# Optimization experiments

Hardware: AMD Instinct MI355X
Metric: run time of the kernel (lower is better)

## Reference

```python
import jax, jax.numpy as jnp
import numpy as np

HIDDEN = 2048
N_HEADS = 16
HEAD_DIM = HIDDEN // N_HEADS  # 128
ROTARY_DIM = 32
ROPE_BASE = 10000.0
NEG_INF = -10000.0  # matches torch code's additive mask constant


def setup_inputs() -> dict:
    key = jax.random.key(0)
    k1, k2, k3 = jax.random.split(key, 3)
    x = jax.random.normal(k1, (2, 2048, HIDDEN), dtype=jnp.float32)
    # scale weights like nn.Linear default init (uniform ~ 1/sqrt(fan_in))
    Wqkv_w = jax.random.normal(k2, (3 * HIDDEN, HIDDEN), dtype=jnp.float32) * (1.0 / np.sqrt(HIDDEN))
    Wqkv_b = jax.random.normal(k3, (3 * HIDDEN,), dtype=jnp.float32) * 0.01
    return {"x": x, "Wqkv_w": Wqkv_w, "Wqkv_b": Wqkv_b}


def _rope_cos_sin(seqlen, dtype):
    inv_freq = 1.0 / (ROPE_BASE ** (jnp.arange(0, ROTARY_DIM, 2, dtype=jnp.float32) / ROTARY_DIM))
    t = jnp.arange(seqlen, dtype=jnp.float32)
    freqs = jnp.outer(t, inv_freq)  # (S, ROTARY_DIM//2)
    return jnp.cos(freqs).astype(dtype), jnp.sin(freqs).astype(dtype)


def _apply_rotary(u, cos, sin):
    # u: (B, S, H, D); rotate first ROTARY_DIM dims, GPT-NeoX half-split style
    u_rot, u_pass = u[..., :ROTARY_DIM], u[..., ROTARY_DIM:]
    u1, u2 = u_rot[..., : ROTARY_DIM // 2], u_rot[..., ROTARY_DIM // 2 :]
    c = cos[None, :, None, :]  # (1, S, 1, ROTARY_DIM//2)
    s = sin[None, :, None, :]
    rot = jnp.concatenate([u1 * c - u2 * s, u1 * s + u2 * c], axis=-1)
    return jnp.concatenate([rot, u_pass], axis=-1)


def reference(x, Wqkv_w, Wqkv_b):
    B, S, _ = x.shape
    qkv = jnp.einsum("bse,oe->bso", x, Wqkv_w) + Wqkv_b  # (B, S, 3*H*D)
    qkv = qkv.reshape(B, S, 3, N_HEADS, HEAD_DIM)
    cos, sin = _rope_cos_sin(S, x.dtype)
    q = _apply_rotary(qkv[:, :, 0], cos, sin)
    k = _apply_rotary(qkv[:, :, 1], cos, sin)
    v = qkv[:, :, 2]
    scale = 1.0 / np.sqrt(HEAD_DIM)
    scores = jnp.einsum("bthd,bshd->bhts", q, k * scale)  # (B, H, T, S)
    causal_mask = jnp.triu(jnp.full((S, S), NEG_INF, dtype=scores.dtype), 1)
    scores = scores + causal_mask
    attn = jax.nn.softmax(scores, axis=-1)
    out = jnp.einsum("bhts,bshd->bthd", attn, v)  # (B, S, H, D)
    return out.reshape(B, S, N_HEADS * HEAD_DIM)
```

## Files before the change

### kernel.cpp

```cpp
#include <hip/hip_runtime.h>

#define B_    2
#define S_    2048
#define E_    2048
#define NH_   16
#define HD_   128
#define NQKV_ 6144
#define M_    4096
#define XN_   (M_ * E_)
#define NPAN  (E_ / 32)

typedef short bf16x8 __attribute__((ext_vector_type(8)));
typedef float f32x4  __attribute__((ext_vector_type(4)));

typedef const __attribute__((address_space(1))) void* gas_t;
typedef __attribute__((address_space(3))) void*       las_t;

__device__ inline float b2f(unsigned short u) {
    return __uint_as_float(((unsigned int)u) << 16);
}
__device__ inline unsigned short f2b(float f) {
    unsigned int x = __float_as_uint(f);
    x = x + 0x7fffu + ((x >> 16) & 1u);
    return (unsigned short)(x >> 16);
}
__device__ inline unsigned int pk2(float lo, float hi) {
    return (unsigned int)f2b(lo) | ((unsigned int)f2b(hi) << 16);
}

__global__ __launch_bounds__(256) void cvt_bf16(
    const float* __restrict__ X,
    const float* __restrict__ W,
    unsigned short* __restrict__ O)
{
    const long i = (long)(blockIdx.x * 256 + threadIdx.x) * 8;
    const float* src = (i < XN_) ? (X + i) : (W + (i - XN_));
    const float4 a = *(const float4*)(src);
    const float4 b = *(const float4*)(src + 4);
    uint4 o = { pk2(a.x, a.y), pk2(a.z, a.w), pk2(b.x, b.y), pk2(b.z, b.w) };
    *(uint4*)(O + i) = o;
}

__global__ __launch_bounds__(512, 2) void qkv_gemm(
    const unsigned short* __restrict__ Xb,
    const unsigned short* __restrict__ Wb,
    const float* __restrict__ bias,
    unsigned short* __restrict__ qb,
    unsigned short* __restrict__ kb,
    unsigned short* __restrict__ vb)
{
    __shared__ __align__(16) unsigned short As[4][256 * 32];
    __shared__ __align__(16) unsigned short Bs[4][256 * 32];

    const int t    = threadIdx.x;
    const int lane = t & 63;
    const int w    = t >> 6;
    const int wr   = w >> 2;
    const int wc   = w & 3;
    const int quad = (lane >> 4) & 3;
    const int l16  = lane & 15;

    const int wg = ((int)blockIdx.x & 7) * 48 + ((int)blockIdx.x >> 3);
    const int m0 = (wg / 24) * 256;
    const int n0 = (wg % 24) * 256;

    auto stageA = [&](int p) {
        const int sl = p & 3;
        const int k0 = p * 32;
        #pragma unroll
        for (int c = 0; c < 2; c++) {
            const int ub  = c * 512 + w * 64;
            const int u   = ub + lane;
            const int row = u >> 2;
            const int ko  = (u & 3) ^ ((row >> 1) & 3);
            __builtin_amdgcn_global_load_lds(
                (gas_t)(Xb + (size_t)(m0 + row) * E_ + k0 + ko * 8),
                (las_t)&As[sl][ub * 8], 16, 0, 0);
        }
    };
    auto stageB = [&](int p) {
        const int sl = p & 3;
        const int k0 = p * 32;
        #pragma unroll
        for (int c = 0; c < 2; c++) {
            const int ub  = c * 512 + w * 64;
            const int u   = ub + lane;
            const int row = u >> 2;
            const int ko  = (u & 3) ^ ((row >> 1) & 3);
            __builtin_amdgcn_global_load_lds(
                (gas_t)(Wb + (size_t)(n0 + row) * E_ + k0 + ko * 8),
                (las_t)&Bs[sl][ub * 8], 16, 0, 0);
        }
    };

    f32x4 acc[8][4];
    #pragma unroll
    for (int i = 0; i < 8; i++)
        #pragma unroll
        for (int j = 0; j < 4; j++)
            #pragma unroll
            for (int r = 0; r < 4; r++) acc[i][j][r] = 0.0f;

    stageA(0); stageB(0);
    stageA(1); stageB(1);
    stageA(2); stageB(2);
    asm volatile("s_waitcnt vmcnt(0)" ::: "memory");
    __builtin_amdgcn_s_barrier();

    for (int p = 0; p < NPAN; p++) {
        const int sl = p & 3;
        bf16x8 af[4], bf[4];

        #pragma unroll
        for (int mf = 0; mf < 4; mf++) {
            const int row = wr * 128 + mf * 16 + l16;
            af[mf] = *(const bf16x8*)&As[sl][row * 32 + (quad ^ ((row >> 1) & 3)) * 8];
        }
        #pragma unroll
        for (int nf = 0; nf < 4; nf++) {
            const int rb = wc * 64 + nf * 16 + l16;
            bf[nf] = *(const bf16x8*)&Bs[sl][rb * 32 + (quad ^ ((rb >> 1) & 3)) * 8];
        }
        if (p + 3 < NPAN) stageA(p + 3);
        __builtin_amdgcn_s_barrier();
        __builtin_amdgcn_s_setprio(1);
        #pragma unroll
        for (int mf = 0; mf < 4; mf++)
            #pragma unroll
            for (int nf = 0; nf < 4; nf++)
                acc[mf][nf] = __builtin_amdgcn_mfma_f32_16x16x32_bf16(
                    af[mf], bf[nf], acc[mf][nf], 0, 0, 0);
        __builtin_amdgcn_s_setprio(0);
        __builtin_amdgcn_s_barrier();

        #pragma unroll
        for (int mf = 0; mf < 4; mf++) {
            const int row = wr * 128 + 64 + mf * 16 + l16;
            af[mf] = *(const bf16x8*)&As[sl][row * 32 + (quad ^ ((row >> 1) & 3)) * 8];
        }
        if (p + 3 < NPAN) stageB(p + 3);
        asm volatile("s_waitcnt vmcnt(8)" ::: "memory");
        __builtin_amdgcn_s_barrier();
        __builtin_amdgcn_s_setprio(1);
        #pragma unroll
        for (int mf = 0; mf < 4; mf++)
            #pragma unroll
            for (int nf = 0; nf < 4; nf++)
                acc[4 + mf][nf] = __builtin_amdgcn_mfma_f32_16x16x32_bf16(
                    af[mf], bf[nf], acc[4 + mf][nf], 0, 0, 0);
        __builtin_amdgcn_s_setprio(0);
        __builtin_amdgcn_s_barrier();
    }

    const int which = n0 >> 11;
    unsigned short* dst = (which == 0) ? qb : ((which == 1) ? kb : vb);

    float bv[4];
    #pragma unroll
    for (int nf = 0; nf < 4; nf++) bv[nf] = bias[n0 + wc * 64 + nf * 16 + l16];
    #pragma unroll
    for (int mi = 0; mi < 8; mi++)
        #pragma unroll
        for (int nf = 0; nf < 4; nf++)
            #pragma unroll
            for (int r = 0; r < 4; r++) acc[mi][nf][r] += bv[nf];

    if ((wc & 1) == 0 && which < 2) {
        const float inv = exp2f(-0.83048202372184059f * (float)l16);
        #pragma unroll
        for (int mi = 0; mi < 8; mi++) {
            #pragma unroll
            for (int r = 0; r < 4; r++) {
                const int m = m0 + wr * 128 + (mi >> 2) * 64 + (mi & 3) * 16
                              + quad * 4 + r;
                const int sdx = m & (S_ - 1);
                float c, sn;
                __sincosf((float)sdx * inv, &sn, &c);
                const float u1 = acc[mi][0][r], u2 = acc[mi][1][r];
                acc[mi][0][r] = u1 * c - u2 * sn;
                acc[mi][1][r] = u1 * sn + u2 * c;
            }
        }
    }

    #pragma unroll
    for (int nf = 0; nf < 4; nf++) {
        const int hh = ((n0 + wc * 64 + nf * 16) >> 7) & 15;
        const int d  = ((wc * 64 + nf * 16) & 127) + l16;
        #pragma unroll
        for (int mi = 0; mi < 8; mi++) {
            #pragma unroll
            for (int r = 0; r < 4; r++) {
                const int m   = m0 + wr * 128 + (mi >> 2) * 64 + (mi & 3) * 16
                                + quad * 4 + r;
                const int bb  = m >> 11;
                const int sdx = m & (S_ - 1);
                dst[((size_t)(bb * NH_ + hh) * S_ + sdx) * HD_ + d] =
                    f2b(acc[mi][nf][r]);
            }
        }
    }
}

#define KSTR 136
#define VSTR 72
#define PSTR 72
#define OSTR 132

__global__ __launch_bounds__(256, 3) void attn_mfma(
    const unsigned short* __restrict__ qb,
    const unsigned short* __restrict__ kb,
    const unsigned short* __restrict__ vb,
    float* __restrict__ out)
{
    union SM {
        struct {
            unsigned short Ks[64 * KSTR];
            unsigned short Vt[128 * VSTR];
            unsigned short Ps[4 * 16 * PSTR];
        } a;
        float Ow[4 * 16 * OSTR];
    };
    __shared__ __align__(16) SM sm;
    unsigned short* Ks = sm.a.Ks;
    unsigned short* Vt = sm.a.Vt;
    unsigned short* Ps = sm.a.Ps;

    const int bid  = blockIdx.x;
    const int qt   = 31 - (bid >> 5);
    const int bh   = bid & 31;
    const int b    = bh >> 4;
    const int h    = bh & 15;
    const int t    = threadIdx.x;
    const int lane = t & 63;
    const int w    = t >> 6;
    const int quad = lane >> 4;
    const int l16  = lane & 15;

    const int wrow0  = qt * 64 + w * 16;
    const int ntiles = qt + 1;

    unsigned short* Pw = Ps + w * 16 * PSTR;

    const int krow = t >> 2, kcb = (t & 3) * 32;
    const int vq   = t & 31, vd0 = (t >> 5) * 16;

    bf16x8 qf[4];
    {
        const unsigned short* qp =
            qb + ((size_t)(bh * S_ + wrow0 + l16)) * HD_ + quad * 8;
        #pragma unroll
        for (int c = 0; c < 4; c++)
            qf[c] = *(const bf16x8*)(qp + c * 32);
    }

    f32x4 of[8];
    #pragma unroll
    for (int db = 0; db < 8; db++)
        #pragma unroll
        for (int r = 0; r < 4; r++) of[db][r] = 0.0f;
    float mr[4], lr[4];
    #pragma unroll
    for (int r = 0; r < 4; r++) { mr[r] = -1e30f; lr[r] = 0.0f; }

    const float scale2 = 0.12751744459892879f;
    const float mneg2  = -14426.950408889634f;

    uint4 kr[4];
    uint4 v0a, v0b, v1a, v1b;

    auto issue_tile = [&](int kt2) {
        const int s2 = kt2 * 64;
        const unsigned short* kg = kb + ((size_t)(bh * S_ + s2 + krow)) * HD_ + kcb;
        #pragma unroll
        for (int u = 0; u < 4; u++) kr[u] = *(const uint4*)(kg + u * 8);
        const unsigned short* vg = vb + ((size_t)(bh * S_ + s2 + 2 * vq)) * HD_ + vd0;
        v0a = *(const uint4*)(vg);
        v0b = *(const uint4*)(vg + 8);
        v1a = *(const uint4*)(vg + HD_);
        v1b = *(const uint4*)(vg + HD_ + 8);
    };

    issue_tile(0);

    for (int kt = 0; kt < ntiles; kt++) {
        const int s0 = kt * 64;
        __syncthreads();
        #pragma unroll
        for (int u = 0; u < 4; u++)
            *(uint4*)&Ks[krow * KSTR + kcb + u * 8] = kr[u];
        {
            unsigned int r0[8] = { v0a.x, v0a.y, v0a.z, v0a.w,
                                   v0b.x, v0b.y, v0b.z, v0b.w };
            unsigned int r1[8] = { v1a.x, v1a.y, v1a.z, v1a.w,
                                   v1b.x, v1b.y, v1b.z, v1b.w };
            #pragma unroll
            for (int j = 0; j < 16; j++) {
                const int u = j >> 1;
                unsigned int pk;
                if ((j & 1) == 0)
                    pk = (r0[u] & 0xffffu) | (r1[u] << 16);
                else
                    pk = (r0[u] >> 16) | (r1[u] & 0xffff0000u);
                *(unsigned int*)&Vt[(vd0 + j) * VSTR + 2 * vq] = pk;
            }
        }
        __syncthreads();

        if (kt + 1 < ntiles) issue_tile(kt + 1);

        f32x4 sf[4];
        #pragma unroll
        for (int nb = 0; nb < 4; nb++)
            #pragma unroll
            for (int r = 0; r < 4; r++) sf[nb][r] = 0.0f;
        #pragma unroll
        for (int c = 0; c < 4; c++) {
            #pragma unroll
            for (int nb = 0; nb < 4; nb++) {
                bf16x8 kf = *(const bf16x8*)&Ks[(nb * 16 + l16) * KSTR + c * 32 + quad * 8];
                sf[nb] = __builtin_amdgcn_mfma_f32_16x16x32_bf16(
                    qf[c], kf, sf[nb], 0, 0, 0);
            }
        }

        const bool need_mask = (s0 + 63 > wrow0);
        {
            const int qr0 = wrow0 + quad * 4;
            #pragma unroll
            for (int nb = 0; nb < 4; nb++) {
                const int kcol = s0 + nb * 16 + l16;
                #pragma unroll
                for (int r = 0; r < 4; r++) {
                    float s = sf[nb][r] * scale2;
                    if (need_mask && kcol > qr0 + r) s += mneg2;
                    sf[nb][r] = s;
                }
            }
        }

        {
            float mt4[4];
            #pragma unroll
            for (int r = 0; r < 4; r++) {
                float mt = fmaxf(fmaxf(sf[0][r], sf[1][r]),
                                 fmaxf(sf[2][r], sf[3][r]));
                mt = fmaxf(mt, __shfl_xor(mt, 1));
                mt = fmaxf(mt, __shfl_xor(mt, 2));
                mt = fmaxf(mt, __shfl_xor(mt, 4));
                mt = fmaxf(mt, __shfl_xor(mt, 8));
                mt4[r] = mt;
            }
            const bool grew = (mt4[0] > mr[0]) || (mt4[1] > mr[1]) ||
                              (mt4[2] > mr[2]) || (mt4[3] > mr[3]);
            if (__any(grew)) {
                float alpha[4];
                #pragma unroll
                for (int r = 0; r < 4; r++) {
                    const float mnew = fmaxf(mr[r], mt4[r]);
                    alpha[r] = __builtin_amdgcn_exp2f(mr[r] - mnew);
                    mr[r] = mnew;
                    lr[r] *= alpha[r];
                }
                #pragma unroll
                for (int db = 0; db < 8; db++)
                    #pragma unroll
                    for (int r = 0; r < 4; r++) of[db][r] *= alpha[r];
            }
            #pragma unroll
            for (int r = 0; r < 4; r++) {
                float rs = 0.0f;
                #pragma unroll
                for (int nb = 0; nb < 4; nb++) {
                    float p = __builtin_amdgcn_exp2f(sf[nb][r] - mr[r]);
                    sf[nb][r] = p;
                    rs += p;
                }
                lr[r] += rs;
            }

            #pragma unroll
            for (int nb = 0; nb < 4; nb++)
                #pragma unroll
                for (int r = 0; r < 4; r++)
                    Pw[(quad * 4 + r) * PSTR + nb * 16 + l16] = f2b(sf[nb][r]);
        }

        #pragma unroll
        for (int kc = 0; kc < 2; kc++) {
            bf16x8 pf = *(const bf16x8*)&Pw[l16 * PSTR + kc * 32 + quad * 8];
            #pragma unroll
            for (int db = 0; db < 8; db++) {
                bf16x8 vf = *(const bf16x8*)&Vt[(db * 16 + l16) * VSTR + kc * 32 + quad * 8];
                of[db] = __builtin_amdgcn_mfma_f32_16x16x32_bf16(
                    pf, vf, of[db], 0, 0, 0);
            }
        }
    }

    float* Ow = sm.Ow + w * 16 * OSTR;
    __syncthreads();
    float inv[4];
    #pragma unroll
    for (int r = 0; r < 4; r++) {
        float ls = lr[r];
        ls += __shfl_xor(ls, 1);
        ls += __shfl_xor(ls, 2);
        ls += __shfl_xor(ls, 4);
        ls += __shfl_xor(ls, 8);
        inv[r] = 1.0f / ls;
    }
    #pragma unroll
    for (int db = 0; db < 8; db++)
        #pragma unroll
        for (int r = 0; r < 4; r++)
            Ow[(quad * 4 + r) * OSTR + db * 16 + l16] = of[db][r] * inv[r];
    #pragma unroll
    for (int rg = 0; rg < 4; rg++) {
        const int rowl = rg * 4 + quad;
        float* op = out + ((size_t)(b * S_ + wrow0 + rowl)) * E_ + h * HD_;
        #pragma unroll
        for (int u = 0; u < 2; u++) {
            float4 v4 = *(const float4*)&Ow[rowl * OSTR + u * 64 + l16 * 4];
            *(float4*)(op + u * 64 + l16 * 4) = v4;
        }
    }
}

extern "C" void kernel_launch(void* const* d_in, const int* in_sizes, int n_in,
                              void* d_out, int out_size, void* d_ws, size_t ws_size,
                              hipStream_t stream)
{
    const float* x    = (const float*)d_in[0];
    const float* W    = (const float*)d_in[1];
    const float* bias = (const float*)d_in[2];
    float* out = (float*)d_out;

    const size_t per = (size_t)B_ * NH_ * S_ * HD_;
    unsigned short* qb = (unsigned short*)d_ws;
    unsigned short* kb = qb + per;
    unsigned short* vb = kb + per;
    unsigned short* Xb = vb + per;
    unsigned short* Wb = Xb + (size_t)XN_;

    const int cvt_elems = XN_ + NQKV_ * E_;
    cvt_bf16<<<cvt_elems / (256 * 8), 256, 0, stream>>>(x, W, Xb);

    dim3 gemm_grid((M_ / 256) * (NQKV_ / 256));
    qkv_gemm<<<gemm_grid, 512, 0, stream>>>(Xb, Wb, bias, qb, kb, vb);

    attn_mfma<<<dim3(32 * 32), 256, 0, stream>>>(qb, kb, vb, out);
}
```

Measured before the change: 372.2 us.

## Shrink QKV GEMM tile and read attention K fragments directly from global

The QKV GEMM tile drops from 256x256 to 128x256, doubling the grid. Its k-loop collapses from two MFMA phases per panel to one, with A and B prefetch issued together and explicit vmcnt waits. In attention, K is no longer staged through shared memory: each wave loads its K fragments straight from global memory. The output staging buffer is halved and written in two passes, cutting LDS use so launch bounds can rise from 3 to 4 blocks per CU. The trade-off is redundant global/L1 traffic for K across the four waves and less data reuse per GEMM block, in exchange for higher occupancy and fewer LDS round trips and barriers.

```diff
diff --git a/kernel.cpp b/kernel.cpp
--- a/kernel.cpp
+++ b/kernel.cpp
@@ -49,7 +49,7 @@
     unsigned short* __restrict__ kb,
     unsigned short* __restrict__ vb)
 {
-    __shared__ __align__(16) unsigned short As[4][256 * 32];
+    __shared__ __align__(16) unsigned short As[4][128 * 32];
     __shared__ __align__(16) unsigned short Bs[4][256 * 32];
 
     const int t    = threadIdx.x;
@@ -60,23 +60,20 @@
     const int quad = (lane >> 4) & 3;
     const int l16  = lane & 15;
 
-    const int wg = ((int)blockIdx.x & 7) * 48 + ((int)blockIdx.x >> 3);
-    const int m0 = (wg / 24) * 256;
+    const int wg = ((int)blockIdx.x & 7) * 96 + ((int)blockIdx.x >> 3);
+    const int m0 = (wg / 24) * 128;
     const int n0 = (wg % 24) * 256;
 
     auto stageA = [&](int p) {
         const int sl = p & 3;
         const int k0 = p * 32;
-        #pragma unroll
-        for (int c = 0; c < 2; c++) {
-            const int ub  = c * 512 + w * 64;
-            const int u   = ub + lane;
-            const int row = u >> 2;
-            const int ko  = (u & 3) ^ ((row >> 1) & 3);
-            __builtin_amdgcn_global_load_lds(
-                (gas_t)(Xb + (size_t)(m0 + row) * E_ + k0 + ko * 8),
-                (las_t)&As[sl][ub * 8], 16, 0, 0);
-        }
+        const int ub  = w * 64;
+        const int u   = ub + lane;
+        const int row = u >> 2;
+        const int ko  = (u & 3) ^ ((row >> 1) & 3);
+        __builtin_amdgcn_global_load_lds(
+            (gas_t)(Xb + (size_t)(m0 + row) * E_ + k0 + ko * 8),
+            (las_t)&As[sl][ub * 8], 16, 0, 0);
     };
     auto stageB = [&](int p) {
         const int sl = p & 3;
@@ -93,9 +90,9 @@
         }
     };
 
-    f32x4 acc[8][4];
-    #pragma unroll
-    for (int i = 0; i < 8; i++)
+    f32x4 acc[4][4];
+    #pragma unroll
+    for (int i = 0; i < 4; i++)
         #pragma unroll
         for (int j = 0; j < 4; j++)
             #pragma unroll
@@ -109,19 +106,27 @@
 
     for (int p = 0; p < NPAN; p++) {
         const int sl = p & 3;
-        bf16x8 af[4], bf[4];
+        bf16x8 af[4], bfv[4];
 
         #pragma unroll
         for (int mf = 0; mf < 4; mf++) {
-            const int row = wr * 128 + mf * 16 + l16;
+            const int row = wr * 64 + mf * 16 + l16;
             af[mf] = *(const bf16x8*)&As[sl][row * 32 + (quad ^ ((row >> 1) & 3)) * 8];
         }
         #pragma unroll
         for (int nf = 0; nf < 4; nf++) {
             const int rb = wc * 64 + nf * 16 + l16;
-            bf[nf] = *(const bf16x8*)&Bs[sl][rb * 32 + (quad ^ ((rb >> 1) & 3)) * 8];
-        }
-        if (p + 3 < NPAN) stageA(p + 3);
+            bfv[nf] = *(const bf16x8*)&Bs[sl][rb * 32 + (quad ^ ((rb >> 1) & 3)) * 8];
+        }
+
+        if (p + 3 < NPAN) {
+            stageA(p + 3); stageB(p + 3);
+            asm volatile("s_waitcnt vmcnt(6)" ::: "memory");
+        } else if (p + 2 < NPAN) {
+            asm volatile("s_waitcnt vmcnt(3)" ::: "memory");
+        } else {
+            asm volatile("s_waitcnt vmcnt(0)" ::: "memory");
+        }
         __builtin_amdgcn_s_barrier();
         __builtin_amdgcn_s_setprio(1);
         #pragma unroll
@@ -129,27 +134,9 @@
             #pragma unroll
             for (int nf = 0; nf < 4; nf++)
                 acc[mf][nf] = __builtin_amdgcn_mfma_f32_16x16x32_bf16(
-                    af[mf], bf[nf], acc[mf][nf], 0, 0, 0);
+                    af[mf], bfv[nf], acc[mf][nf], 0, 0, 0);
         __builtin_amdgcn_s_setprio(0);
         __builtin_amdgcn_s_barrier();
-
-        #pragma unroll
-        for (int mf = 0; mf < 4; mf++) {
-            const int row = wr * 128 + 64 + mf * 16 + l16;
-            af[mf] = *(const bf16x8*)&As[sl][row * 32 + (quad ^ ((row >> 1) & 3)) * 8];
-        }
-        if (p + 3 < NPAN) stageB(p + 3);
-        asm volatile("s_waitcnt vmcnt(8)" ::: "memory");
-        __builtin_amdgcn_s_barrier();
-        __builtin_amdgcn_s_setprio(1);
-        #pragma unroll
-        for (int mf = 0; mf < 4; mf++)
-            #pragma unroll
-            for (int nf = 0; nf < 4; nf++)
-                acc[4 + mf][nf] = __builtin_amdgcn_mfma_f32_16x16x32_bf16(
-                    af[mf], bf[nf], acc[4 + mf][nf], 0, 0, 0);
-        __builtin_amdgcn_s_setprio(0);
-        __builtin_amdgcn_s_barrier();
     }
 
     const int which = n0 >> 11;
@@ -159,7 +146,7 @@
     #pragma unroll
     for (int nf = 0; nf < 4; nf++) bv[nf] = bias[n0 + wc * 64 + nf * 16 + l16];
     #pragma unroll
-    for (int mi = 0; mi < 8; mi++)
+    for (int mi = 0; mi < 4; mi++)
         #pragma unroll
         for (int nf = 0; nf < 4; nf++)
             #pragma unroll
@@ -168,11 +155,10 @@
     if ((wc & 1) == 0 && which < 2) {
         const float inv = exp2f(-0.83048202372184059f * (float)l16);
         #pragma unroll
-        for (int mi = 0; mi < 8; mi++) {
+        for (int mi = 0; mi < 4; mi++) {
             #pragma unroll
             for (int r = 0; r < 4; r++) {
-                const int m = m0 + wr * 128 + (mi >> 2) * 64 + (mi & 3) * 16
-                              + quad * 4 + r;
+                const int m = m0 + wr * 64 + mi * 16 + quad * 4 + r;
                 const int sdx = m & (S_ - 1);
                 float c, sn;
                 __sincosf((float)sdx * inv, &sn, &c);
@@ -188,11 +174,10 @@
         const int hh = ((n0 + wc * 64 + nf * 16) >> 7) & 15;
         const int d  = ((wc * 64 + nf * 16) & 127) + l16;
         #pragma unroll
-        for (int mi = 0; mi < 8; mi++) {
+        for (int mi = 0; mi < 4; mi++) {
             #pragma unroll
             for (int r = 0; r < 4; r++) {
-                const int m   = m0 + wr * 128 + (mi >> 2) * 64 + (mi & 3) * 16
-                                + quad * 4 + r;
+                const int m   = m0 + wr * 64 + mi * 16 + quad * 4 + r;
                 const int bb  = m >> 11;
                 const int sdx = m & (S_ - 1);
                 dst[((size_t)(bb * NH_ + hh) * S_ + sdx) * HD_ + d] =
@@ -202,12 +187,11 @@
     }
 }
 
-#define KSTR 136
 #define VSTR 72
 #define PSTR 72
-#define OSTR 132
-
-__global__ __launch_bounds__(256, 3) void attn_mfma(
+#define OSTR 68
+
+__global__ __launch_bounds__(256, 4) void attn_mfma(
     const unsigned short* __restrict__ qb,
     const unsigned short* __restrict__ kb,
     const unsigned short* __restrict__ vb,
@@ -215,14 +199,12 @@
 {
     union SM {
         struct {
-            unsigned short Ks[64 * KSTR];
             unsigned short Vt[128 * VSTR];
             unsigned short Ps[4 * 16 * PSTR];
         } a;
         float Ow[4 * 16 * OSTR];
     };
     __shared__ __align__(16) SM sm;
-    unsigned short* Ks = sm.a.Ks;
     unsigned short* Vt = sm.a.Vt;
     unsigned short* Ps = sm.a.Ps;
 
@@ -242,8 +224,7 @@
 
     unsigned short* Pw = Ps + w * 16 * PSTR;
 
-    const int krow = t >> 2, kcb = (t & 3) * 32;
-    const int vq   = t & 31, vd0 = (t >> 5) * 16;
+    const int vq = t & 31, vd0 = (t >> 5) * 16;
 
     bf16x8 qf[4];
     {
@@ -254,6 +235,9 @@
             qf[c] = *(const bf16x8*)(qp + c * 32);
     }
 
+    const unsigned short* kgb =
+        kb + ((size_t)(bh * S_)) * HD_ + quad * 8;
+
     f32x4 of[8];
     #pragma unroll
     for (int db = 0; db < 8; db++)
@@ -266,14 +250,10 @@
     const float scale2 = 0.12751744459892879f;
     const float mneg2  = -14426.950408889634f;
 
-    uint4 kr[4];
     uint4 v0a, v0b, v1a, v1b;
 
     auto issue_tile = [&](int kt2) {
         const int s2 = kt2 * 64;
-        const unsigned short* kg = kb + ((size_t)(bh * S_ + s2 + krow)) * HD_ + kcb;
-        #pragma unroll
-        for (int u = 0; u < 4; u++) kr[u] = *(const uint4*)(kg + u * 8);
         const unsigned short* vg = vb + ((size_t)(bh * S_ + s2 + 2 * vq)) * HD_ + vd0;
         v0a = *(const uint4*)(vg);
         v0b = *(const uint4*)(vg + 8);
@@ -286,9 +266,6 @@
     for (int kt = 0; kt < ntiles; kt++) {
         const int s0 = kt * 64;
         __syncthreads();
-        #pragma unroll
-        for (int u = 0; u < 4; u++)
-            *(uint4*)&Ks[krow * KSTR + kcb + u * 8] = kr[u];
         {
             unsigned int r0[8] = { v0a.x, v0a.y, v0a.z, v0a.w,
                                    v0b.x, v0b.y, v0b.z, v0b.w };
@@ -314,13 +291,18 @@
         for (int nb = 0; nb < 4; nb++)
             #pragma unroll
             for (int r = 0; r < 4; r++) sf[nb][r] = 0.0f;
-        #pragma unroll
-        for (int c = 0; c < 4; c++) {
-            #pragma unroll
-            for (int nb = 0; nb < 4; nb++) {
-                bf16x8 kf = *(const bf16x8*)&Ks[(nb * 16 + l16) * KSTR + c * 32 + quad * 8];
-                sf[nb] = __builtin_amdgcn_mfma_f32_16x16x32_bf16(
-                    qf[c], kf, sf[nb], 0, 0, 0);
+        {
+            const unsigned short* kg = kgb + (size_t)(s0 + l16) * HD_;
+            #pragma unroll
+            for (int c = 0; c < 4; c++) {
+                bf16x8 kf[4];
+                #pragma unroll
+                for (int nb = 0; nb < 4; nb++)
+                    kf[nb] = *(const bf16x8*)(kg + (size_t)(nb * 16) * HD_ + c * 32);
+                #pragma unroll
+                for (int nb = 0; nb < 4; nb++)
+                    sf[nb] = __builtin_amdgcn_mfma_f32_16x16x32_bf16(
+                        qf[c], kf[nb], sf[nb], 0, 0, 0);
             }
         }
 
@@ -411,18 +393,20 @@
         inv[r] = 1.0f / ls;
     }
     #pragma unroll
-    for (int db = 0; db < 8; db++)
-        #pragma unroll
-        for (int r = 0; r < 4; r++)
-            Ow[(quad * 4 + r) * OSTR + db * 16 + l16] = of[db][r] * inv[r];
-    #pragma unroll
-    for (int rg = 0; rg < 4; rg++) {
-        const int rowl = rg * 4 + quad;
-        float* op = out + ((size_t)(b * S_ + wrow0 + rowl)) * E_ + h * HD_;
-        #pragma unroll
-        for (int u = 0; u < 2; u++) {
-            float4 v4 = *(const float4*)&Ow[rowl * OSTR + u * 64 + l16 * 4];
-            *(float4*)(op + u * 64 + l16 * 4) = v4;
+    for (int half = 0; half < 2; half++) {
+        #pragma unroll
+        for (int db4 = 0; db4 < 4; db4++) {
+            const int db = half * 4 + db4;
+            #pragma unroll
+            for (int r = 0; r < 4; r++)
+                Ow[(quad * 4 + r) * OSTR + db4 * 16 + l16] = of[db][r] * inv[r];
+        }
+        #pragma unroll
+        for (int rg = 0; rg < 4; rg++) {
+            const int rowl = rg * 4 + quad;
+            float* op = out + ((size_t)(b * S_ + wrow0 + rowl)) * E_ + h * HD_;
+            float4 v4 = *(const float4*)&Ow[rowl * OSTR + l16 * 4];
+            *(float4*)(op + half * 64 + l16 * 4) = v4;
         }
     }
 }
@@ -446,7 +430,7 @@
     const int cvt_elems = XN_ + NQKV_ * E_;
     cvt_bf16<<<cvt_elems / (256 * 8), 256, 0, stream>>>(x, W, Xb);
 
-    dim3 gemm_grid((M_ / 256) * (NQKV_ / 256));
+    dim3 gemm_grid((M_ / 128) * (NQKV_ / 256));
     qkv_gemm<<<gemm_grid, 512, 0, stream>>>(Xb, Wb, bias, qb, kb, vb);
 
     attn_mfma<<<dim3(32 * 32), 256, 0, stream>>>(qb, kb, vb, out);
```

After: 471.6 us. +26.7%, slower.
